# Kernel optimization log

Hardware: AMD Instinct MI355X
Metric: run time of the kernel (lower is better)

## Reference

```python
import jax, jax.numpy as jnp
import numpy as np

B, DZ, M_, N_ = 2048, 256, 64, 64
GAMMA, EPS, MAXITERS = 1.0, 1e-6, 1000


def sinkhorn(Mcost):
    # entropic OT with uniform marginals r=1/m, c=1/n (ddn sinkhorn, non-logspace)
    b, h, w = Mcost.shape
    r = 1.0 / h
    c = 1.0 / w
    P = jnp.exp(-GAMMA * Mcost)
    P = P / jnp.sum(P, axis=(1, 2), keepdims=True)

    def cond_fn(state):
        P, it, err = state
        return jnp.logical_and(it < MAXITERS, err > EPS)

    def body_fn(state):
        P, it, _ = state
        alpha = jnp.sum(P, axis=2, keepdims=True)   # row sums (B,h,1)
        P = P * (r / alpha)                          # row normalize to r
        beta = jnp.sum(P, axis=1, keepdims=True)    # col sums (B,1,w)
        err = jnp.max(jnp.abs(beta - c))
        # torch loop breaks BEFORE col-normalizing when converged
        P = jnp.where(err <= EPS, P, P * (c / beta))
        return P, it + 1, err

    init_err = jnp.array(jnp.inf, dtype=Mcost.dtype)
    P, _, _ = jax.lax.while_loop(cond_fn, body_fn, (P, jnp.array(0, jnp.int32), init_err))
    return P


def setup_inputs() -> dict:
    key = jax.random.key(0)
    ks = jax.random.split(key, 7)
    H = M_ * N_
    z = jax.random.normal(ks[0], (B, DZ), dtype=jnp.float32)
    W1 = jax.random.normal(ks[1], (DZ, H), dtype=jnp.float32) * (1.0 / np.sqrt(DZ))
    b1 = jnp.zeros((H,), jnp.float32)
    W2 = jax.random.normal(ks[2], (H, H), dtype=jnp.float32) * (1.0 / np.sqrt(H))
    b2 = jnp.zeros((H,), jnp.float32)
    W3 = jax.random.normal(ks[3], (H, H), dtype=jnp.float32) * (1.0 / np.sqrt(H))
    b3 = jnp.zeros((H,), jnp.float32)
    return {"z": z, "W1": W1, "b1": b1, "W2": W2, "b2": b2, "W3": W3, "b3": b3}


def reference(z, W1, b1, W2, b2, W3, b3):
    x = jax.nn.relu(z @ W1 + b1)
    x = jax.nn.relu(x @ W2 + b2)
    x = x @ W3 + b3
    x = x.reshape(z.shape[0], M_, N_)  # (B, m, n) cost matrix
    return sinkhorn(x)
```

## Files before the change

### kernel.cpp

```cpp
#include <hip/hip_runtime.h>
#include <hip/hip_bf16.h>

typedef unsigned short ushort_t;
typedef __attribute__((ext_vector_type(8))) short bf16x8;
typedef __attribute__((ext_vector_type(4))) float f32x4;

#define MDIM 2048
#define NDIM 4096

__device__ __forceinline__ ushort_t to_bf16(float f) {
    __hip_bfloat16 h = __float2bfloat16(f);
    return *reinterpret_cast<ushort_t*>(&h);
}

__global__ void cast_bf16_kernel(const float* __restrict__ in, ushort_t* __restrict__ out, int n) {
    int i = blockIdx.x * blockDim.x + threadIdx.x;
    if (i < n) out[i] = to_bf16(in[i]);
}

__global__ void transpose_cast_kernel(const float* __restrict__ W, ushort_t* __restrict__ WT,
                                      int K, int N) {
    __shared__ float tile[32][33];
    const int tx = threadIdx.x, ty = threadIdx.y;
    const int n0 = blockIdx.x * 32, k0 = blockIdx.y * 32;
#pragma unroll
    for (int r = 0; r < 4; ++r)
        tile[ty + r * 8][tx] = W[(size_t)(k0 + ty + r * 8) * N + n0 + tx];
    __syncthreads();
    const int t = ty * 32 + tx;
    const int nl = t >> 3;
    const int kc = (t & 7) * 4;
    ushort4 o;
    o.x = to_bf16(tile[kc + 0][nl]);
    o.y = to_bf16(tile[kc + 1][nl]);
    o.z = to_bf16(tile[kc + 2][nl]);
    o.w = to_bf16(tile[kc + 3][nl]);
    *reinterpret_cast<ushort4*>(&WT[(size_t)(n0 + nl) * K + k0 + kc]) = o;
}


#define GLD(gp, lp) __builtin_amdgcn_global_load_lds(                      \
        (const __attribute__((address_space(1))) void*)(gp),               \
        (__attribute__((address_space(3))) void*)(lp), 16, 0, 0)

#define MFMA(d, a, b) d = __builtin_amdgcn_mfma_f32_16x16x32_bf16(a, b, d, 0, 0, 0)

template <typename OutT, bool RELU>
__global__ __launch_bounds__(512, 2) void gemm_p8(const ushort_t* __restrict__ A,
                                                  const ushort_t* __restrict__ BT,
                                                  const float* __restrict__ bias,
                                                  OutT* __restrict__ C, int Kdim) {
    __shared__ __align__(16) ushort_t As[3][128 * 64];
    __shared__ __align__(16) ushort_t Bs[3][256 * 64];

    const int t = threadIdx.x;
    const int l = t & 63;
    const int w = t >> 6;
    const int l16 = l & 15;
    const int quad = l >> 4;
    const int wr = w >> 2;
    const int wc = w & 3;
    const int m0 = blockIdx.y * 128;
    const int n0 = blockIdx.x * 256;

    f32x4 acc[4][4];
#pragma unroll
    for (int i = 0; i < 4; ++i)
#pragma unroll
        for (int j = 0; j < 4; ++j) acc[i][j] = (f32x4){0.f, 0.f, 0.f, 0.f};

    const int srow = w * 8 + (l >> 3);
    const int scol = ((l & 7) ^ (l >> 3)) * 8;
    const ushort_t* gA0 = A  + (size_t)(m0 + srow) * Kdim + scol;
    const ushort_t* gA1 = A  + (size_t)(m0 + 64 + srow) * Kdim + scol;
    const ushort_t* gB0 = BT + (size_t)(n0 + srow) * Kdim + scol;
    const ushort_t* gB1 = BT + (size_t)(n0 + 64 + srow) * Kdim + scol;
    const ushort_t* gB2 = BT + (size_t)(n0 + 128 + srow) * Kdim + scol;
    const ushort_t* gB3 = BT + (size_t)(n0 + 192 + srow) * Kdim + scol;
    const int ldsW = w * 8 * 64;

    const int swz = l16 & 7;
#define LDA_(base, i, kk) (*(const bf16x8*)&(base)[(wr * 64 + (i) * 16 + l16) * 64 + ((((kk) * 4 + quad) ^ swz) * 8)])
#define LDB_(base, j, kk) (*(const bf16x8*)&(base)[(wc * 64 + (j) * 16 + l16) * 64 + ((((kk) * 4 + quad) ^ swz) * 8)])

#define STAGE_TILE(buf, koff) do {                      \
        GLD(gA0 + (koff), &As[buf][ldsW]);              \
        GLD(gA1 + (koff), &As[buf][ldsW + 64 * 64]);    \
        GLD(gB0 + (koff), &Bs[buf][ldsW]);              \
        GLD(gB1 + (koff), &Bs[buf][ldsW + 64 * 64]);    \
        GLD(gB2 + (koff), &Bs[buf][ldsW + 128 * 64]);   \
        GLD(gB3 + (koff), &Bs[buf][ldsW + 192 * 64]);   \
    } while (0)

#define MFMA16(a0, a1, a2, a3, b0, b1, b2, b3)                     \
        MFMA(acc[0][0], a0, b0); MFMA(acc[0][1], a0, b1);          \
        MFMA(acc[0][2], a0, b2); MFMA(acc[0][3], a0, b3);          \
        MFMA(acc[1][0], a1, b0); MFMA(acc[1][1], a1, b1);          \
        MFMA(acc[1][2], a1, b2); MFMA(acc[1][3], a1, b3);          \
        MFMA(acc[2][0], a2, b0); MFMA(acc[2][1], a2, b1);          \
        MFMA(acc[2][2], a2, b2); MFMA(acc[2][3], a2, b3);          \
        MFMA(acc[3][0], a3, b0); MFMA(acc[3][1], a3, b1);          \
        MFMA(acc[3][2], a3, b2); MFMA(acc[3][3], a3, b3)

    const int nt = Kdim >> 6;

    STAGE_TILE(0, 0);
    STAGE_TILE(1, 64);
    asm volatile("s_waitcnt vmcnt(6)" ::: "memory");
    __builtin_amdgcn_s_barrier();

    for (int tt = 0; tt < nt; ++tt) {
        const int buf = tt % 3;
        const int nb = (tt + 2) % 3;
        const int koff = (tt + 2) << 6;
        const bool more = (tt + 2) < nt;

        const ushort_t* __restrict__ Ab = &As[buf][0];
        const ushort_t* __restrict__ Bb = &Bs[buf][0];

        bf16x8 a00 = LDA_(Ab, 0, 0), a01 = LDA_(Ab, 1, 0), a02 = LDA_(Ab, 2, 0), a03 = LDA_(Ab, 3, 0);
        bf16x8 b00 = LDB_(Bb, 0, 0), b01 = LDB_(Bb, 1, 0), b02 = LDB_(Bb, 2, 0), b03 = LDB_(Bb, 3, 0);
        bf16x8 a10 = LDA_(Ab, 0, 1), a11 = LDA_(Ab, 1, 1), a12 = LDA_(Ab, 2, 1), a13 = LDA_(Ab, 3, 1);
        bf16x8 b10 = LDB_(Bb, 0, 1), b11 = LDB_(Bb, 1, 1), b12 = LDB_(Bb, 2, 1), b13 = LDB_(Bb, 3, 1);

        if (more) STAGE_TILE(nb, koff);

        MFMA16(a00, a01, a02, a03, b00, b01, b02, b03);
        MFMA16(a10, a11, a12, a13, b10, b11, b12, b13);

        if (tt + 1 < nt) {
            if (more) asm volatile("s_waitcnt vmcnt(6)" ::: "memory");
            else      asm volatile("s_waitcnt vmcnt(0)" ::: "memory");
            __builtin_amdgcn_s_barrier();
        }
    }

#pragma unroll
    for (int i = 0; i < 4; ++i) {
#pragma unroll
        for (int r = 0; r < 4; ++r) {
            const int grow = m0 + wr * 64 + i * 16 + quad * 4 + r;
#pragma unroll
            for (int j = 0; j < 4; ++j) {
                const int gcol = n0 + wc * 64 + j * 16 + l16;
                float v = acc[i][j][r] + bias[gcol];
                if (RELU) v = fmaxf(v, 0.0f);
                if constexpr (sizeof(OutT) == 2) {
                    C[(size_t)grow * NDIM + gcol] = to_bf16(v);
                } else {
                    C[(size_t)grow * NDIM + gcol] = v;
                }
            }
        }
    }
}

__device__ __forceinline__ float rdl(float v, int l) {
    return __uint_as_float(__builtin_amdgcn_readlane(__float_as_uint(v), l));
}

__global__ __launch_bounds__(64) void sinkhorn_kernel(float* __restrict__ PM) {
    __shared__ __align__(16) float T[64 * 65];
    const int l = threadIdx.x;
    float* base = PM + (size_t)blockIdx.x * 4096;

    float Kcol[64];
    float Krow[64];
#pragma unroll
    for (int r = 0; r < 64; ++r)
        Kcol[r] = __expf(-base[r * 64 + l]);
#pragma unroll
    for (int r = 0; r < 64; ++r)
        T[r * 65 + l] = Kcol[r];
    __syncthreads();
#pragma unroll
    for (int c = 0; c < 64; ++c)
        Krow[c] = T[l * 65 + c];

    float a = 0.0f, b = 1.0f;
    for (int it = 0; it < 1000; ++it) {
        float t1 = 0.0f;
#pragma unroll
        for (int c = 0; c < 64; ++c)
            t1 = fmaf(Krow[c], rdl(b, c), t1);
        a = 0.015625f / t1;

        float t2 = 0.0f;
#pragma unroll
        for (int r = 0; r < 64; ++r)
            t2 = fmaf(Kcol[r], rdl(a, r), t2);
        const float err = fabsf(b * t2 - 0.015625f);
        if (__ballot(err > 1e-6f) == 0ull) break;
        b = 0.015625f / t2;
    }

#pragma unroll
    for (int r = 0; r < 64; ++r)
        base[r * 64 + l] = rdl(a, r) * Kcol[r] * b;
}

extern "C" void kernel_launch(void* const* d_in, const int* in_sizes, int n_in,
                              void* d_out, int out_size, void* d_ws, size_t ws_size,
                              hipStream_t stream) {
    const float* z  = (const float*)d_in[0];
    const float* W1 = (const float*)d_in[1];
    const float* b1 = (const float*)d_in[2];
    const float* W2 = (const float*)d_in[3];
    const float* b2 = (const float*)d_in[4];
    const float* W3 = (const float*)d_in[5];
    const float* b3 = (const float*)d_in[6];
    float* out = (float*)d_out;
    char* ws = (char*)d_ws;

    ushort_t* W2T = (ushort_t*)(ws + 0);
    ushort_t* W3T = (ushort_t*)(ws + (size_t)33554432);
    ushort_t* C1b = (ushort_t*)(ws + (size_t)67108864);
    ushort_t* C2b = (ushort_t*)(ws + (size_t)83886080);
    ushort_t* Zb  = (ushort_t*)(ws + (size_t)100663296);
    ushort_t* W1T = (ushort_t*)(ws + (size_t)101711872);

    cast_bf16_kernel<<<2048, 256, 0, stream>>>(z, Zb, MDIM * 256);
    transpose_cast_kernel<<<dim3(128, 8), dim3(32, 8), 0, stream>>>(W1, W1T, 256, 4096);
    transpose_cast_kernel<<<dim3(128, 128), dim3(32, 8), 0, stream>>>(W2, W2T, 4096, 4096);
    transpose_cast_kernel<<<dim3(128, 128), dim3(32, 8), 0, stream>>>(W3, W3T, 4096, 4096);

    gemm_p8<ushort_t, true><<<dim3(NDIM / 256, MDIM / 128), 512, 0, stream>>>(Zb, W1T, b1, C1b, 256);
    gemm_p8<ushort_t, true><<<dim3(NDIM / 256, MDIM / 128), 512, 0, stream>>>(C1b, W2T, b2, C2b, 4096);
    gemm_p8<float, false><<<dim3(NDIM / 256, MDIM / 128), 512, 0, stream>>>(C2b, W3T, b3, out, 4096);

    sinkhorn_kernel<<<2048, 64, 0, stream>>>(out);
}
```

Baseline: 333.0 us.

## Use 4 waves per GEMM block with 64x128 per-wave tiles

Halves the GEMM block to 256 threads (4 waves in a 2x2 grid), so each wave computes a 64x128 output tile with 32 accumulators instead of 64x64. Each thread now issues 12 global-to-LDS loads per stage instead of 6, and the wait counts are adjusted to match. The goal is more MFMA work per LDS fragment load and fewer waves to synchronise. The cost is far more accumulator and fragment registers per wave, and launch bounds of 1 block per CU, which lowers occupancy and latency hiding.

```diff
diff --git a/kernel.cpp b/kernel.cpp
--- a/kernel.cpp
+++ b/kernel.cpp
@@ -46,7 +46,7 @@
 #define MFMA(d, a, b) d = __builtin_amdgcn_mfma_f32_16x16x32_bf16(a, b, d, 0, 0, 0)
 
 template <typename OutT, bool RELU>
-__global__ __launch_bounds__(512, 2) void gemm_p8(const ushort_t* __restrict__ A,
+__global__ __launch_bounds__(256, 1) void gemm_p8(const ushort_t* __restrict__ A,
                                                   const ushort_t* __restrict__ BT,
                                                   const float* __restrict__ bias,
                                                   OutT* __restrict__ C, int Kdim) {
@@ -58,55 +58,48 @@
     const int w = t >> 6;
     const int l16 = l & 15;
     const int quad = l >> 4;
-    const int wr = w >> 2;
-    const int wc = w & 3;
+    const int wr = w >> 1;
+    const int wc = w & 1;
     const int m0 = blockIdx.y * 128;
     const int n0 = blockIdx.x * 256;
 
-    f32x4 acc[4][4];
+    f32x4 acc[4][8];
 #pragma unroll
     for (int i = 0; i < 4; ++i)
 #pragma unroll
-        for (int j = 0; j < 4; ++j) acc[i][j] = (f32x4){0.f, 0.f, 0.f, 0.f};
+        for (int j = 0; j < 8; ++j) acc[i][j] = (f32x4){0.f, 0.f, 0.f, 0.f};
 
     const int srow = w * 8 + (l >> 3);
     const int scol = ((l & 7) ^ (l >> 3)) * 8;
-    const ushort_t* gA0 = A  + (size_t)(m0 + srow) * Kdim + scol;
-    const ushort_t* gA1 = A  + (size_t)(m0 + 64 + srow) * Kdim + scol;
-    const ushort_t* gB0 = BT + (size_t)(n0 + srow) * Kdim + scol;
-    const ushort_t* gB1 = BT + (size_t)(n0 + 64 + srow) * Kdim + scol;
-    const ushort_t* gB2 = BT + (size_t)(n0 + 128 + srow) * Kdim + scol;
-    const ushort_t* gB3 = BT + (size_t)(n0 + 192 + srow) * Kdim + scol;
+    const ushort_t* gA = A  + (size_t)(m0 + srow) * Kdim + scol;
+    const ushort_t* gB = BT + (size_t)(n0 + srow) * Kdim + scol;
     const int ldsW = w * 8 * 64;
+    const size_t rstep = (size_t)32 * Kdim;
+
+#define STAGE_TILE(buf, koff) do {                                   \
+        GLD(gA + (koff),             &As[buf][ldsW]);                \
+        GLD(gA + (koff) + rstep,     &As[buf][ldsW + 32 * 64]);      \
+        GLD(gA + (koff) + 2 * rstep, &As[buf][ldsW + 64 * 64]);      \
+        GLD(gA + (koff) + 3 * rstep, &As[buf][ldsW + 96 * 64]);      \
+        GLD(gB + (koff),             &Bs[buf][ldsW]);                \
+        GLD(gB + (koff) + rstep,     &Bs[buf][ldsW + 32 * 64]);      \
+        GLD(gB + (koff) + 2 * rstep, &Bs[buf][ldsW + 64 * 64]);      \
+        GLD(gB + (koff) + 3 * rstep, &Bs[buf][ldsW + 96 * 64]);      \
+        GLD(gB + (koff) + 4 * rstep, &Bs[buf][ldsW + 128 * 64]);     \
+        GLD(gB + (koff) + 5 * rstep, &Bs[buf][ldsW + 160 * 64]);     \
+        GLD(gB + (koff) + 6 * rstep, &Bs[buf][ldsW + 192 * 64]);     \
+        GLD(gB + (koff) + 7 * rstep, &Bs[buf][ldsW + 224 * 64]);     \
+    } while (0)
 
     const int swz = l16 & 7;
 #define LDA_(base, i, kk) (*(const bf16x8*)&(base)[(wr * 64 + (i) * 16 + l16) * 64 + ((((kk) * 4 + quad) ^ swz) * 8)])
-#define LDB_(base, j, kk) (*(const bf16x8*)&(base)[(wc * 64 + (j) * 16 + l16) * 64 + ((((kk) * 4 + quad) ^ swz) * 8)])
-
-#define STAGE_TILE(buf, koff) do {                      \
-        GLD(gA0 + (koff), &As[buf][ldsW]);              \
-        GLD(gA1 + (koff), &As[buf][ldsW + 64 * 64]);    \
-        GLD(gB0 + (koff), &Bs[buf][ldsW]);              \
-        GLD(gB1 + (koff), &Bs[buf][ldsW + 64 * 64]);    \
-        GLD(gB2 + (koff), &Bs[buf][ldsW + 128 * 64]);   \
-        GLD(gB3 + (koff), &Bs[buf][ldsW + 192 * 64]);   \
-    } while (0)
-
-#define MFMA16(a0, a1, a2, a3, b0, b1, b2, b3)                     \
-        MFMA(acc[0][0], a0, b0); MFMA(acc[0][1], a0, b1);          \
-        MFMA(acc[0][2], a0, b2); MFMA(acc[0][3], a0, b3);          \
-        MFMA(acc[1][0], a1, b0); MFMA(acc[1][1], a1, b1);          \
-        MFMA(acc[1][2], a1, b2); MFMA(acc[1][3], a1, b3);          \
-        MFMA(acc[2][0], a2, b0); MFMA(acc[2][1], a2, b1);          \
-        MFMA(acc[2][2], a2, b2); MFMA(acc[2][3], a2, b3);          \
-        MFMA(acc[3][0], a3, b0); MFMA(acc[3][1], a3, b1);          \
-        MFMA(acc[3][2], a3, b2); MFMA(acc[3][3], a3, b3)
+#define LDB_(base, j, kk) (*(const bf16x8*)&(base)[(wc * 128 + (j) * 16 + l16) * 64 + ((((kk) * 4 + quad) ^ swz) * 8)])
 
     const int nt = Kdim >> 6;
 
     STAGE_TILE(0, 0);
     STAGE_TILE(1, 64);
-    asm volatile("s_waitcnt vmcnt(6)" ::: "memory");
+    asm volatile("s_waitcnt vmcnt(12)" ::: "memory");
     __builtin_amdgcn_s_barrier();
 
     for (int tt = 0; tt < nt; ++tt) {
@@ -118,18 +111,27 @@
         const ushort_t* __restrict__ Ab = &As[buf][0];
         const ushort_t* __restrict__ Bb = &Bs[buf][0];
 
-        bf16x8 a00 = LDA_(Ab, 0, 0), a01 = LDA_(Ab, 1, 0), a02 = LDA_(Ab, 2, 0), a03 = LDA_(Ab, 3, 0);
-        bf16x8 b00 = LDB_(Bb, 0, 0), b01 = LDB_(Bb, 1, 0), b02 = LDB_(Bb, 2, 0), b03 = LDB_(Bb, 3, 0);
-        bf16x8 a10 = LDA_(Ab, 0, 1), a11 = LDA_(Ab, 1, 1), a12 = LDA_(Ab, 2, 1), a13 = LDA_(Ab, 3, 1);
-        bf16x8 b10 = LDB_(Bb, 0, 1), b11 = LDB_(Bb, 1, 1), b12 = LDB_(Bb, 2, 1), b13 = LDB_(Bb, 3, 1);
+        bf16x8 af[2][4], bfr[2][8];
+#pragma unroll
+        for (int kk = 0; kk < 2; ++kk) {
+#pragma unroll
+            for (int i = 0; i < 4; ++i) af[kk][i] = LDA_(Ab, i, kk);
+#pragma unroll
+            for (int j = 0; j < 8; ++j) bfr[kk][j] = LDB_(Bb, j, kk);
+        }
 
         if (more) STAGE_TILE(nb, koff);
 
-        MFMA16(a00, a01, a02, a03, b00, b01, b02, b03);
-        MFMA16(a10, a11, a12, a13, b10, b11, b12, b13);
+#pragma unroll
+        for (int kk = 0; kk < 2; ++kk)
+#pragma unroll
+            for (int i = 0; i < 4; ++i)
+#pragma unroll
+                for (int j = 0; j < 8; ++j)
+                    MFMA(acc[i][j], af[kk][i], bfr[kk][j]);
 
         if (tt + 1 < nt) {
-            if (more) asm volatile("s_waitcnt vmcnt(6)" ::: "memory");
+            if (more) asm volatile("s_waitcnt vmcnt(12)" ::: "memory");
             else      asm volatile("s_waitcnt vmcnt(0)" ::: "memory");
             __builtin_amdgcn_s_barrier();
         }
@@ -141,8 +143,8 @@
         for (int r = 0; r < 4; ++r) {
             const int grow = m0 + wr * 64 + i * 16 + quad * 4 + r;
 #pragma unroll
-            for (int j = 0; j < 4; ++j) {
-                const int gcol = n0 + wc * 64 + j * 16 + l16;
+            for (int j = 0; j < 8; ++j) {
+                const int gcol = n0 + wc * 128 + j * 16 + l16;
                 float v = acc[i][j][r] + bias[gcol];
                 if (RELU) v = fmaxf(v, 0.0f);
                 if constexpr (sizeof(OutT) == 2) {
@@ -224,9 +226,9 @@
     transpose_cast_kernel<<<dim3(128, 128), dim3(32, 8), 0, stream>>>(W2, W2T, 4096, 4096);
     transpose_cast_kernel<<<dim3(128, 128), dim3(32, 8), 0, stream>>>(W3, W3T, 4096, 4096);
 
-    gemm_p8<ushort_t, true><<<dim3(NDIM / 256, MDIM / 128), 512, 0, stream>>>(Zb, W1T, b1, C1b, 256);
-    gemm_p8<ushort_t, true><<<dim3(NDIM / 256, MDIM / 128), 512, 0, stream>>>(C1b, W2T, b2, C2b, 4096);
-    gemm_p8<float, false><<<dim3(NDIM / 256, MDIM / 128), 512, 0, stream>>>(C2b, W3T, b3, out, 4096);
+    gemm_p8<ushort_t, true><<<dim3(NDIM / 256, MDIM / 128), 256, 0, stream>>>(Zb, W1T, b1, C1b, 256);
+    gemm_p8<ushort_t, true><<<dim3(NDIM / 256, MDIM / 128), 256, 0, stream>>>(C1b, W2T, b2, C2b, 4096);
+    gemm_p8<float, false><<<dim3(NDIM / 256, MDIM / 128), 256, 0, stream>>>(C2b, W3T, b3, out, 4096);
 
     sinkhorn_kernel<<<2048, 64, 0, stream>>>(out);
 }
```

Result: slower. 361.8 us (+8.6%).
